# Kernel tuning notes

Hardware: AMD Instinct MI355X
Metric: run time of the kernel (lower is better)

## Reference

```python
import jax, jax.numpy as jnp
import numpy as np

B, L, D, H = 8, 256, 512, 512
NEG_BIG = 1e8  # matches the 100000000.0 mask constant in the original


def setup_inputs() -> dict:
    key = jax.random.key(0)
    k1, k2, k3, k4 = jax.random.split(key, 4)
    enc = jax.random.normal(k1, (B, L, D), dtype=jnp.float32)
    # Glorot-uniform init, matching tf.keras.initializers.GlorotUniform
    s_w = float(np.sqrt(6.0 / (D + H)))
    W_l = jax.random.uniform(k2, (D, H), jnp.float32, -s_w, s_w)
    W_r = jax.random.uniform(k3, (D, H), jnp.float32, -s_w, s_w)
    s_u = float(np.sqrt(6.0 / (H + H)))  # 1-D glorot: fan_in = fan_out = H
    U = jax.random.uniform(k4, (H,), jnp.float32, -s_u, s_u)
    logit_bias = jnp.zeros((1,), jnp.float32)  # bias_initial_value=None -> zeros init
    return {"encoder_output": enc, "W_l": W_l, "W_r": W_r, "U": U, "logit_bias": logit_bias}


def reference(encoder_output, W_l, W_r, U, logit_bias):
    # dot_l[b,i,h], dot_r[b,j,h]
    dot_l = jnp.einsum('bik,kh->bih', encoder_output, W_l)
    dot_r = jnp.einsum('bjk,kh->bjh', encoder_output, W_r)
    # additive biaffine: tanh(dot_l_i + dot_r_j) . U  -> logits[b,i,j]
    final_sum = jnp.tanh(dot_l[:, :, None, :] + dot_r[:, None, :, :])  # [B,L,L,H]
    logits = jnp.einsum('bijh,h->bij', final_sum, U) + logit_bias[0]   # [B,L,L]
    # per-row self-mask (one_hot(i)) applied over all rows at once
    masked = logits - NEG_BIG * jnp.eye(L, dtype=logits.dtype)[None]   # [B,L,L]
    # original returns python lists over i of [B,L]; stack -> [L,B,L]
    mask_scores = jnp.transpose(masked, (1, 0, 2))
    p = jax.nn.sigmoid(mask_scores)
    samples = jax.random.bernoulli(jax.random.key(42), p).astype(jnp.int32)  # [L,B,L]
    # Bernoulli entropy from logits x: p*softplus(-x) + (1-p)*softplus(x)
    entropy = p * jax.nn.softplus(-mask_scores) + (1.0 - p) * jax.nn.softplus(mask_scores)
    return samples, mask_scores, entropy
```

## Files before the change

kernel.cpp:

```cpp
#include <hip/hip_runtime.h>
#include <stdint.h>

#define Bb 8
#define Ll 256
#define Dd 512
#define Hh 512
#define Nout (Ll * Bb * Ll)

#define Kc 2.8853900817779268

#define RNG_PARTITIONABLE 1

__device__ __forceinline__ uint32_t rotl32(uint32_t v, int s) {
  return (v << s) | (v >> (32 - s));
}
__device__ __forceinline__ void tf_round(uint32_t& x0, uint32_t& x1, int r) {
  x0 += x1;
  x1 = rotl32(x1, r);
  x1 ^= x0;
}
__device__ __forceinline__ uint2 threefry2x32_k042(uint32_t x0, uint32_t x1) {
  const uint32_t k0 = 0u;
  const uint32_t k1 = 42u;
  const uint32_t k2 = 0x1BD11BDAu ^ k0 ^ k1;
  x0 += k0; x1 += k1;
  tf_round(x0, x1, 13); tf_round(x0, x1, 15); tf_round(x0, x1, 26); tf_round(x0, x1, 6);
  x0 += k1; x1 += k2 + 1u;
  tf_round(x0, x1, 17); tf_round(x0, x1, 29); tf_round(x0, x1, 16); tf_round(x0, x1, 24);
  x0 += k2; x1 += k0 + 2u;
  tf_round(x0, x1, 13); tf_round(x0, x1, 15); tf_round(x0, x1, 26); tf_round(x0, x1, 6);
  x0 += k0; x1 += k1 + 3u;
  tf_round(x0, x1, 17); tf_round(x0, x1, 29); tf_round(x0, x1, 16); tf_round(x0, x1, 24);
  x0 += k1; x1 += k2 + 4u;
  tf_round(x0, x1, 13); tf_round(x0, x1, 15); tf_round(x0, x1, 26); tf_round(x0, x1, 6);
  x0 += k2; x1 += k0 + 5u;
  return make_uint2(x0, x1);
}

__device__ __forceinline__ uint32_t rng_bits(uint32_t n) {
#if RNG_PARTITIONABLE
  uint2 o = threefry2x32_k042(0u, n);
  return o.x ^ o.y;
#else
  const uint32_t half = (uint32_t)(Nout / 2);
  if (n < half) {
    uint2 o = threefry2x32_k042(n, n + half);
    return o.x;
  } else {
    uint2 o = threefry2x32_k042(n - half, n);
    return o.y;
  }
#endif
}

__global__ __launch_bounds__(256) void gemm_proj(
    const float* __restrict__ enc, const float* __restrict__ Wl,
    const float* __restrict__ Wr, float* __restrict__ el,
    float* __restrict__ er) {
  const float* W = (blockIdx.z == 0) ? Wl : Wr;
  float* C = (blockIdx.z == 0) ? el : er;
  const int m0 = blockIdx.x * 64;
  const int n0 = blockIdx.y * 64;

  __shared__ float As[2][32][68];
  __shared__ float Ws[2][32][68];

  const int t = threadIdx.x;
  const int tx = t & 15;
  const int ty = t >> 4;

  double accd[4][4];
#pragma unroll
  for (int r = 0; r < 4; ++r)
#pragma unroll
    for (int c = 0; c < 4; ++c) accd[r][c] = 0.0;

  float4 pa[2], pw[2];
#pragma unroll
  for (int r = 0; r < 2; ++r) {
    const int idx = t + r * 256;
    const int am = idx >> 3, akq = idx & 7;
    pa[r] = *(const float4*)(enc + (size_t)(m0 + am) * Dd + akq * 4);
    const int wk = idx >> 4, wnq = idx & 15;
    pw[r] = *(const float4*)(W + (size_t)wk * Hh + n0 + wnq * 4);
  }
#pragma unroll
  for (int r = 0; r < 2; ++r) {
    const int idx = t + r * 256;
    const int am = idx >> 3, akq = idx & 7;
    As[0][akq * 4 + 0][am] = pa[r].x;
    As[0][akq * 4 + 1][am] = pa[r].y;
    As[0][akq * 4 + 2][am] = pa[r].z;
    As[0][akq * 4 + 3][am] = pa[r].w;
    const int wk = idx >> 4, wnq = idx & 15;
    *(float4*)&Ws[0][wk][wnq * 4] = pw[r];
  }
  __syncthreads();

  for (int s = 0; s < 16; ++s) {
    const int buf = s & 1;
    if (s < 15) {
      const int k0 = (s + 1) * 32;
#pragma unroll
      for (int r = 0; r < 2; ++r) {
        const int idx = t + r * 256;
        const int am = idx >> 3, akq = idx & 7;
        pa[r] = *(const float4*)(enc + (size_t)(m0 + am) * Dd + k0 + akq * 4);
        const int wk = idx >> 4, wnq = idx & 15;
        pw[r] = *(const float4*)(W + (size_t)(k0 + wk) * Hh + n0 + wnq * 4);
      }
    }

    float accf[4][4];
#pragma unroll
    for (int r = 0; r < 4; ++r)
#pragma unroll
      for (int c = 0; c < 4; ++c) accf[r][c] = 0.0f;

#pragma unroll
    for (int k = 0; k < 32; ++k) {
      const float4 av = *(const float4*)&As[buf][k][ty * 4];
      const float4 bv = *(const float4*)&Ws[buf][k][tx * 4];
      accf[0][0] = __builtin_fmaf(av.x, bv.x, accf[0][0]);
      accf[0][1] = __builtin_fmaf(av.x, bv.y, accf[0][1]);
      accf[0][2] = __builtin_fmaf(av.x, bv.z, accf[0][2]);
      accf[0][3] = __builtin_fmaf(av.x, bv.w, accf[0][3]);
      accf[1][0] = __builtin_fmaf(av.y, bv.x, accf[1][0]);
      accf[1][1] = __builtin_fmaf(av.y, bv.y, accf[1][1]);
      accf[1][2] = __builtin_fmaf(av.y, bv.z, accf[1][2]);
      accf[1][3] = __builtin_fmaf(av.y, bv.w, accf[1][3]);
      accf[2][0] = __builtin_fmaf(av.z, bv.x, accf[2][0]);
      accf[2][1] = __builtin_fmaf(av.z, bv.y, accf[2][1]);
      accf[2][2] = __builtin_fmaf(av.z, bv.z, accf[2][2]);
      accf[2][3] = __builtin_fmaf(av.z, bv.w, accf[2][3]);
      accf[3][0] = __builtin_fmaf(av.w, bv.x, accf[3][0]);
      accf[3][1] = __builtin_fmaf(av.w, bv.y, accf[3][1]);
      accf[3][2] = __builtin_fmaf(av.w, bv.z, accf[3][2]);
      accf[3][3] = __builtin_fmaf(av.w, bv.w, accf[3][3]);
    }
#pragma unroll
    for (int r = 0; r < 4; ++r)
#pragma unroll
      for (int c = 0; c < 4; ++c) accd[r][c] += (double)accf[r][c];

    if (s < 15) {
      const int nb = buf ^ 1;
#pragma unroll
      for (int r = 0; r < 2; ++r) {
        const int idx = t + r * 256;
        const int am = idx >> 3, akq = idx & 7;
        As[nb][akq * 4 + 0][am] = pa[r].x;
        As[nb][akq * 4 + 1][am] = pa[r].y;
        As[nb][akq * 4 + 2][am] = pa[r].z;
        As[nb][akq * 4 + 3][am] = pa[r].w;
        const int wk = idx >> 4, wnq = idx & 15;
        *(float4*)&Ws[nb][wk][wnq * 4] = pw[r];
      }
    }
    __syncthreads();
  }

#pragma unroll
  for (int r = 0; r < 4; ++r) {
    float4 v;
    v.x = __builtin_amdgcn_exp2f((float)(Kc * accd[r][0]));
    v.y = __builtin_amdgcn_exp2f((float)(Kc * accd[r][1]));
    v.z = __builtin_amdgcn_exp2f((float)(Kc * accd[r][2]));
    v.w = __builtin_amdgcn_exp2f((float)(Kc * accd[r][3]));
    *(float4*)(C + (size_t)(m0 + ty * 4 + r) * Hh + n0 + tx * 4) = v;
  }
}

__device__ __forceinline__ void group4_acc(float& S, const float4 a,
                                           const float4 bv, const float4 u) {
  const float d0 = __builtin_fmaf(a.x, bv.x, 1.0f);
  const float d1 = __builtin_fmaf(a.y, bv.y, 1.0f);
  const float d2 = __builtin_fmaf(a.z, bv.z, 1.0f);
  const float d3 = __builtin_fmaf(a.w, bv.w, 1.0f);
  const float p01 = d0 * d1;
  const float p23 = d2 * d3;
  const float D = p01 * p23;
  float n01 = u.x * d1;
  n01 = __builtin_fmaf(u.y, d0, n01);
  float n23 = u.z * d3;
  n23 = __builtin_fmaf(u.w, d2, n23);
  float num = n01 * p23;
  num = __builtin_fmaf(n23, p01, num);
  S = __builtin_fmaf(num, __builtin_amdgcn_rcpf(D), S);
}

__global__ __launch_bounds__(256) void biaffine_part(
    const float* __restrict__ el, const float* __restrict__ er,
    const float* __restrict__ U, float* __restrict__ part) {
  const int zz = blockIdx.z;
  const int b = zz & 7;
  const int ks = zz >> 3;
  const int i0 = blockIdx.y * 64;
  const int j0 = blockIdx.x * 64;
  const int h0 = ks * 64;

  __shared__ float els[64][68];
  __shared__ float ers[64][68];
  __shared__ float us[64];

  const int t = threadIdx.x;
  if (t < 16) *(float4*)&us[t * 4] = *(const float4*)(U + h0 + t * 4);

  const float* elg = el + (size_t)(b * Ll + i0) * Hh + h0;
  const float* erg = er + (size_t)(b * Ll + j0) * Hh + h0;
#pragma unroll
  for (int rep = 0; rep < 4; ++rep) {
    const int idx = t + rep * 256;
    const int r = idx >> 4;
    const int c = (idx & 15) * 4;
    *(float4*)&els[r][c] = *(const float4*)(elg + (size_t)r * Hh + c);
    *(float4*)&ers[r][c] = *(const float4*)(erg + (size_t)r * Hh + c);
  }
  __syncthreads();

  float usl = 0.0f;
#pragma unroll
  for (int q = 0; q < 16; ++q) {
    const float4 u = *(const float4*)&us[q * 4];
    usl += ((u.x + u.y) + u.z) + u.w;
  }

  const int ti = t >> 4;
  const int tj = t & 15;

  float S[4][4];
#pragma unroll
  for (int r = 0; r < 4; ++r)
#pragma unroll
    for (int c = 0; c < 4; ++c) S[r][c] = 0.0f;

#pragma unroll 2
  for (int g = 0; g < 16; ++g) {
    const int h = g * 4;
    const float4 u = *(const float4*)&us[h];
    float4 av[4], bv[4];
#pragma unroll
    for (int c = 0; c < 4; ++c) {
      av[c] = *(const float4*)&els[ti + 16 * c][h];
      bv[c] = *(const float4*)&ers[tj + 16 * c][h];
    }
#pragma unroll
    for (int r = 0; r < 4; ++r)
#pragma unroll
      for (int c = 0; c < 4; ++c) group4_acc(S[r][c], av[r], bv[c], u);
  }

  float* pslice = part + (size_t)ks * Nout;
#pragma unroll
  for (int r = 0; r < 4; ++r) {
    const int i = i0 + ti + 16 * r;
#pragma unroll
    for (int c = 0; c < 4; ++c) {
      const int j = j0 + tj + 16 * c;
      const uint32_t n = ((uint32_t)i * Bb + (uint32_t)b) * Ll + (uint32_t)j;
      pslice[n] = __builtin_fmaf(-2.0f, S[r][c], usl);
    }
  }
}

__global__ __launch_bounds__(256) void biaffine_emit(
    const float* __restrict__ part, const float* __restrict__ biasp,
    float* __restrict__ out) {
  const uint32_t n4 = (blockIdx.x * 256u + threadIdx.x) * 4u;
  double s0 = 0.0, s1 = 0.0, s2 = 0.0, s3 = 0.0;
#pragma unroll
  for (int k = 0; k < 8; ++k) {
    const float4 v = *(const float4*)(part + (size_t)k * Nout + n4);
    s0 += (double)v.x;
    s1 += (double)v.y;
    s2 += (double)v.z;
    s3 += (double)v.w;
  }
  const float bias = biasp[0];
  const double sv[4] = {s0, s1, s2, s3};

  float4 samp4, x4, ent4;
  float* sp = &samp4.x;
  float* xp = &x4.x;
  float* ep = &ent4.x;
#pragma unroll
  for (int q = 0; q < 4; ++q) {
    const uint32_t n = n4 + q;
    const int i = (int)(n >> 11);
    const int j = (int)(n & 255u);
    float x = (float)sv[q] + bias;
    if (i == j) x -= 1e8f;

    const double pd = 1.0 / (1.0 + exp(-(double)x));
    const float pf = (float)pd;

    const uint32_t bits = rng_bits(n);
    const float uu = __uint_as_float((bits >> 9) | 0x3f800000u) - 1.0f;
    sp[q] = (uu < pf) ? 1.0f : 0.0f;
    xp[q] = x;

    const float ax = fabsf(x);
    const float l1p = log1pf(expf(-ax));
    const float sp_pos = fmaxf(x, 0.0f) + l1p;
    const float sp_neg = fmaxf(-x, 0.0f) + l1p;
    ep[q] = pf * sp_neg + (1.0f - pf) * sp_pos;
  }
  *(float4*)(out + n4) = samp4;
  *(float4*)(out + Nout + n4) = x4;
  *(float4*)(out + 2 * (size_t)Nout + n4) = ent4;
}

extern "C" void kernel_launch(void* const* d_in, const int* in_sizes, int n_in,
                              void* d_out, int out_size, void* d_ws,
                              size_t ws_size, hipStream_t stream) {
  const float* enc = (const float*)d_in[0];
  const float* Wl = (const float*)d_in[1];
  const float* Wr = (const float*)d_in[2];
  const float* U = (const float*)d_in[3];
  const float* lb = (const float*)d_in[4];
  float* out = (float*)d_out;

  float* el = (float*)d_ws;
  float* er = el + (size_t)Bb * Ll * Hh;
  float* part = er + (size_t)Bb * Ll * Hh;

  gemm_proj<<<dim3(2048 / 64, Hh / 64, 2), 256, 0, stream>>>(enc, Wl, Wr, el, er);
  biaffine_part<<<dim3(Ll / 64, Ll / 64, Bb * 8), 256, 0, stream>>>(el, er, U, part);
  biaffine_emit<<<dim3(Nout / 1024), 256, 0, stream>>>(part, lb, out);
}
```

Measured before the change: 130.8 us.

## Replace fp32 projection GEMM with split-bf16 MFMA GEMM

```diff
diff --git a/kernel.cpp b/kernel.cpp
--- a/kernel.cpp
+++ b/kernel.cpp
@@ -10,6 +10,9 @@
 #define Kc 2.8853900817779268
 
 #define RNG_PARTITIONABLE 1
+
+typedef __attribute__((ext_vector_type(8))) short bf16x8;
+typedef __attribute__((ext_vector_type(4))) float f32x4;
 
 __device__ __forceinline__ uint32_t rotl32(uint32_t v, int s) {
   return (v << s) | (v >> (32 - s));
@@ -53,121 +56,138 @@
 #endif
 }
 
-__global__ __launch_bounds__(256) void gemm_proj(
-    const float* __restrict__ enc, const float* __restrict__ Wl,
-    const float* __restrict__ Wr, float* __restrict__ el,
-    float* __restrict__ er) {
-  const float* W = (blockIdx.z == 0) ? Wl : Wr;
-  float* C = (blockIdx.z == 0) ? el : er;
-  const int m0 = blockIdx.x * 64;
+__device__ __forceinline__ unsigned short bf16_rne(float f) {
+  uint32_t u = __float_as_uint(f);
+  u = (u + 0x7fffu + ((u >> 16) & 1u)) >> 16;
+  return (unsigned short)u;
+}
+__device__ __forceinline__ float bf16_tof(unsigned short h) {
+  return __uint_as_float(((uint32_t)h) << 16);
+}
+__device__ __forceinline__ void split3(float a, unsigned short& h,
+                                       unsigned short& m, unsigned short& l) {
+  h = bf16_rne(a);
+  const float r1 = a - bf16_tof(h);
+  m = bf16_rne(r1);
+  const float r2 = r1 - bf16_tof(m);
+  l = bf16_rne(r2);
+}
+
+__global__ __launch_bounds__(256) void split_enc(
+    const float* __restrict__ enc, unsigned short* __restrict__ ah,
+    unsigned short* __restrict__ am, unsigned short* __restrict__ al) {
+  const int idx = (blockIdx.x * 256 + threadIdx.x) * 4;
+  const float4 v = *(const float4*)(enc + idx);
+  ushort4 h4, m4, l4;
+  split3(v.x, h4.x, m4.x, l4.x);
+  split3(v.y, h4.y, m4.y, l4.y);
+  split3(v.z, h4.z, m4.z, l4.z);
+  split3(v.w, h4.w, m4.w, l4.w);
+  *(ushort4*)(ah + idx) = h4;
+  *(ushort4*)(am + idx) = m4;
+  *(ushort4*)(al + idx) = l4;
+}
+
+__global__ __launch_bounds__(256) void split_wt(
+    const float* __restrict__ Wl, const float* __restrict__ Wr,
+    unsigned short* __restrict__ wh, unsigned short* __restrict__ wm,
+    unsigned short* __restrict__ wl) {
+  const int z = blockIdx.z;
+  const float* W = z ? Wr : Wl;
+  const size_t zo = (size_t)z * Hh * Dd;
+  const int k0 = blockIdx.x * 64;
   const int n0 = blockIdx.y * 64;
-
-  __shared__ float As[2][32][68];
-  __shared__ float Ws[2][32][68];
+  __shared__ float tile[64][65];
 
   const int t = threadIdx.x;
-  const int tx = t & 15;
-  const int ty = t >> 4;
-
-  double accd[4][4];
-#pragma unroll
-  for (int r = 0; r < 4; ++r)
-#pragma unroll
-    for (int c = 0; c < 4; ++c) accd[r][c] = 0.0;
-
-  float4 pa[2], pw[2];
-#pragma unroll
-  for (int r = 0; r < 2; ++r) {
-    const int idx = t + r * 256;
-    const int am = idx >> 3, akq = idx & 7;
-    pa[r] = *(const float4*)(enc + (size_t)(m0 + am) * Dd + akq * 4);
-    const int wk = idx >> 4, wnq = idx & 15;
-    pw[r] = *(const float4*)(W + (size_t)wk * Hh + n0 + wnq * 4);
-  }
-#pragma unroll
-  for (int r = 0; r < 2; ++r) {
-    const int idx = t + r * 256;
-    const int am = idx >> 3, akq = idx & 7;
-    As[0][akq * 4 + 0][am] = pa[r].x;
-    As[0][akq * 4 + 1][am] = pa[r].y;
-    As[0][akq * 4 + 2][am] = pa[r].z;
-    As[0][akq * 4 + 3][am] = pa[r].w;
-    const int wk = idx >> 4, wnq = idx & 15;
-    *(float4*)&Ws[0][wk][wnq * 4] = pw[r];
+#pragma unroll
+  for (int rep = 0; rep < 4; ++rep) {
+    const int idx = t + rep * 256;
+    const int r = idx >> 4;
+    const int c = (idx & 15) * 4;
+    const float4 v = *(const float4*)(W + (size_t)(k0 + r) * Hh + n0 + c);
+    tile[r][c + 0] = v.x; tile[r][c + 1] = v.y;
+    tile[r][c + 2] = v.z; tile[r][c + 3] = v.w;
   }
   __syncthreads();
-
-  for (int s = 0; s < 16; ++s) {
-    const int buf = s & 1;
-    if (s < 15) {
-      const int k0 = (s + 1) * 32;
-#pragma unroll
-      for (int r = 0; r < 2; ++r) {
-        const int idx = t + r * 256;
-        const int am = idx >> 3, akq = idx & 7;
-        pa[r] = *(const float4*)(enc + (size_t)(m0 + am) * Dd + k0 + akq * 4);
-        const int wk = idx >> 4, wnq = idx & 15;
-        pw[r] = *(const float4*)(W + (size_t)(k0 + wk) * Hh + n0 + wnq * 4);
-      }
+#pragma unroll
+  for (int rep = 0; rep < 4; ++rep) {
+    const int idx = t + rep * 256;
+    const int rr = idx >> 4;
+    const int cc = (idx & 15) * 4;
+    ushort4 h4, m4, l4;
+    split3(tile[cc + 0][rr], h4.x, m4.x, l4.x);
+    split3(tile[cc + 1][rr], h4.y, m4.y, l4.y);
+    split3(tile[cc + 2][rr], h4.z, m4.z, l4.z);
+    split3(tile[cc + 3][rr], h4.w, m4.w, l4.w);
+    const size_t o = zo + (size_t)(n0 + rr) * Dd + k0 + cc;
+    *(ushort4*)(wh + o) = h4;
+    *(ushort4*)(wm + o) = m4;
+    *(ushort4*)(wl + o) = l4;
+  }
+}
+
+__global__ __launch_bounds__(256) void gemm_mfma(
+    const unsigned short* __restrict__ ah, const unsigned short* __restrict__ am,
+    const unsigned short* __restrict__ al, const unsigned short* __restrict__ wh,
+    const unsigned short* __restrict__ wm, const unsigned short* __restrict__ wl,
+    float* __restrict__ el, float* __restrict__ er) {
+  const int z = blockIdx.z;
+  const size_t zo = (size_t)z * Hh * Dd;
+  float* C = z ? er : el;
+
+  const int lane = threadIdx.x & 63;
+  const int wv = threadIdx.x >> 6;
+  const int m0 = blockIdx.x * 64 + wv * 16;
+  const int n0 = blockIdx.y * 64;
+
+  const int l15 = lane & 15;
+  const int kq = (lane >> 4) * 8;
+
+  const size_t a_off = (size_t)(m0 + l15) * Dd + kq;
+  size_t b_off[4];
+#pragma unroll
+  for (int nt = 0; nt < 4; ++nt)
+    b_off[nt] = zo + (size_t)(n0 + nt * 16 + l15) * Dd + kq;
+
+  f32x4 acc[4][2];
+#pragma unroll
+  for (int nt = 0; nt < 4; ++nt)
+#pragma unroll
+    for (int hf = 0; hf < 2; ++hf) acc[nt][hf] = (f32x4){0.f, 0.f, 0.f, 0.f};
+
+  for (int kc = 0; kc < 16; ++kc) {
+    const int k0 = kc * 32;
+    const bf16x8 a_h = *(const bf16x8*)(ah + a_off + k0);
+    const bf16x8 a_m = *(const bf16x8*)(am + a_off + k0);
+    const bf16x8 a_l = *(const bf16x8*)(al + a_off + k0);
+    const int hf = kc >> 3;
+#pragma unroll
+    for (int nt = 0; nt < 4; ++nt) {
+      const bf16x8 b_h = *(const bf16x8*)(wh + b_off[nt] + k0);
+      const bf16x8 b_m = *(const bf16x8*)(wm + b_off[nt] + k0);
+      const bf16x8 b_l = *(const bf16x8*)(wl + b_off[nt] + k0);
+      f32x4 A = acc[nt][hf];
+      A = __builtin_amdgcn_mfma_f32_16x16x32_bf16(a_h, b_h, A, 0, 0, 0);
+      A = __builtin_amdgcn_mfma_f32_16x16x32_bf16(a_h, b_m, A, 0, 0, 0);
+      A = __builtin_amdgcn_mfma_f32_16x16x32_bf16(a_m, b_h, A, 0, 0, 0);
+      A = __builtin_amdgcn_mfma_f32_16x16x32_bf16(a_h, b_l, A, 0, 0, 0);
+      A = __builtin_amdgcn_mfma_f32_16x16x32_bf16(a_l, b_h, A, 0, 0, 0);
+      A = __builtin_amdgcn_mfma_f32_16x16x32_bf16(a_m, b_m, A, 0, 0, 0);
+      acc[nt][hf] = A;
     }
-
-    float accf[4][4];
-#pragma unroll
-    for (int r = 0; r < 4; ++r)
-#pragma unroll
-      for (int c = 0; c < 4; ++c) accf[r][c] = 0.0f;
-
-#pragma unroll
-    for (int k = 0; k < 32; ++k) {
-      const float4 av = *(const float4*)&As[buf][k][ty * 4];
-      const float4 bv = *(const float4*)&Ws[buf][k][tx * 4];
-      accf[0][0] = __builtin_fmaf(av.x, bv.x, accf[0][0]);
-      accf[0][1] = __builtin_fmaf(av.x, bv.y, accf[0][1]);
-      accf[0][2] = __builtin_fmaf(av.x, bv.z, accf[0][2]);
-      accf[0][3] = __builtin_fmaf(av.x, bv.w, accf[0][3]);
-      accf[1][0] = __builtin_fmaf(av.y, bv.x, accf[1][0]);
-      accf[1][1] = __builtin_fmaf(av.y, bv.y, accf[1][1]);
-      accf[1][2] = __builtin_fmaf(av.y, bv.z, accf[1][2]);
-      accf[1][3] = __builtin_fmaf(av.y, bv.w, accf[1][3]);
-      accf[2][0] = __builtin_fmaf(av.z, bv.x, accf[2][0]);
-      accf[2][1] = __builtin_fmaf(av.z, bv.y, accf[2][1]);
-      accf[2][2] = __builtin_fmaf(av.z, bv.z, accf[2][2]);
-      accf[2][3] = __builtin_fmaf(av.z, bv.w, accf[2][3]);
-      accf[3][0] = __builtin_fmaf(av.w, bv.x, accf[3][0]);
-      accf[3][1] = __builtin_fmaf(av.w, bv.y, accf[3][1]);
-      accf[3][2] = __builtin_fmaf(av.w, bv.z, accf[3][2]);
-      accf[3][3] = __builtin_fmaf(av.w, bv.w, accf[3][3]);
+  }
+
+  const int rbase = (lane >> 4) * 4;
+#pragma unroll
+  for (int nt = 0; nt < 4; ++nt) {
+    const int n = n0 + nt * 16 + l15;
+#pragma unroll
+    for (int reg = 0; reg < 4; ++reg) {
+      const double s = (double)acc[nt][0][reg] + (double)acc[nt][1][reg];
+      const int m = m0 + rbase + reg;
+      C[(size_t)m * Hh + n] = __builtin_amdgcn_exp2f((float)(Kc * s));
     }
-#pragma unroll
-    for (int r = 0; r < 4; ++r)
-#pragma unroll
-      for (int c = 0; c < 4; ++c) accd[r][c] += (double)accf[r][c];
-
-    if (s < 15) {
-      const int nb = buf ^ 1;
-#pragma unroll
-      for (int r = 0; r < 2; ++r) {
-        const int idx = t + r * 256;
-        const int am = idx >> 3, akq = idx & 7;
-        As[nb][akq * 4 + 0][am] = pa[r].x;
-        As[nb][akq * 4 + 1][am] = pa[r].y;
-        As[nb][akq * 4 + 2][am] = pa[r].z;
-        As[nb][akq * 4 + 3][am] = pa[r].w;
-        const int wk = idx >> 4, wnq = idx & 15;
-        *(float4*)&Ws[nb][wk][wnq * 4] = pw[r];
-      }
-    }
-    __syncthreads();
-  }
-
-#pragma unroll
-  for (int r = 0; r < 4; ++r) {
-    float4 v;
-    v.x = __builtin_amdgcn_exp2f((float)(Kc * accd[r][0]));
-    v.y = __builtin_amdgcn_exp2f((float)(Kc * accd[r][1]));
-    v.z = __builtin_amdgcn_exp2f((float)(Kc * accd[r][2]));
-    v.w = __builtin_amdgcn_exp2f((float)(Kc * accd[r][3]));
-    *(float4*)(C + (size_t)(m0 + ty * 4 + r) * Hh + n0 + tx * 4) = v;
   }
 }
 
@@ -234,7 +254,6 @@
 #pragma unroll
     for (int c = 0; c < 4; ++c) S[r][c] = 0.0f;
 
-#pragma unroll 2
   for (int g = 0; g < 16; ++g) {
     const int h = g * 4;
     const float4 u = *(const float4*)&us[h];
@@ -320,11 +339,21 @@
   const float* lb = (const float*)d_in[4];
   float* out = (float*)d_out;
 
-  float* el = (float*)d_ws;
-  float* er = el + (size_t)Bb * Ll * Hh;
-  float* part = er + (size_t)Bb * Ll * Hh;
-
-  gemm_proj<<<dim3(2048 / 64, Hh / 64, 2), 256, 0, stream>>>(enc, Wl, Wr, el, er);
+  char* w = (char*)d_ws;
+  float* el = (float*)w;                      w += (size_t)Bb * Ll * Hh * 4;
+  float* er = (float*)w;                      w += (size_t)Bb * Ll * Hh * 4;
+  float* part = (float*)w;                    w += (size_t)8 * Nout * 4;
+  unsigned short* ah = (unsigned short*)w;    w += (size_t)Bb * Ll * Dd * 2;
+  unsigned short* am = (unsigned short*)w;    w += (size_t)Bb * Ll * Dd * 2;
+  unsigned short* al = (unsigned short*)w;    w += (size_t)Bb * Ll * Dd * 2;
+  unsigned short* wh = (unsigned short*)w;    w += (size_t)2 * Dd * Hh * 2;
+  unsigned short* wm = (unsigned short*)w;    w += (size_t)2 * Dd * Hh * 2;
+  unsigned short* wl = (unsigned short*)w;    w += (size_t)2 * Dd * Hh * 2;
+
+  split_enc<<<dim3((Bb * Ll * Dd) / 1024), 256, 0, stream>>>(enc, ah, am, al);
+  split_wt<<<dim3(Dd / 64, Hh / 64, 2), 256, 0, stream>>>(Wl, Wr, wh, wm, wl);
+  gemm_mfma<<<dim3((Bb * Ll) / 64, Hh / 64, 2), 256, 0, stream>>>(
+      ah, am, al, wh, wm, wl, el, er);
   biaffine_part<<<dim3(Ll / 64, Ll / 64, Bb * 8), 256, 0, stream>>>(el, er, U, part);
   biaffine_emit<<<dim3(Nout / 1024), 256, 0, stream>>>(part, lb, out);
 }
```

Result: slower. 157.1 us (+20.2%).
